# Kernel tuning notes

Measured on AMD Instinct MI355X. Metric: run time of the kernel, lower is better.

## Reference

```python
import jax, jax.numpy as jnp
import numpy as np
from math import sqrt

NUM_ENT = 100000
NUM_REL = 237  # base; rel table has 2*NUM_REL rows
DIM = 200
HALF = DIM // 2


def _lrelu(x, slope):
    return jnp.where(x >= 0, x, slope * x)


def setup_inputs() -> dict:
    key = jax.random.key(0)
    ks = jax.random.split(key, 20)
    s = 0.02
    inp = {
        'edge_index': jax.random.randint(ks[0], (2, 500000), 0, NUM_ENT),
        'edge_type': jax.random.randint(ks[1], (500000,), 0, 2 * NUM_REL),
        'toTest': jax.random.randint(ks[2], (131072, 2), 0, NUM_ENT),
        'ent_emb': s * jax.random.normal(ks[3], (NUM_ENT, DIM), jnp.float32),
        'rel_emb': s * jax.random.normal(ks[4], (2 * NUM_REL, DIM), jnp.float32),
        'W': s * jax.random.normal(ks[5], (DIM, DIM), jnp.float32),
        'W_loop': s * jax.random.normal(ks[6], (DIM, DIM), jnp.float32),
        'W_rel': s * jax.random.normal(ks[7], (DIM, DIM), jnp.float32),
        'trans_w': s * jax.random.normal(ks[8], (DIM, HALF), jnp.float32),
        'trans_b': jnp.zeros((HALF,), jnp.float32),
        'q_w': s * jax.random.normal(ks[9], (HALF, 128), jnp.float32),
        'q_b': jnp.zeros((128,), jnp.float32),
        'k_w': s * jax.random.normal(ks[10], (HALF, 128), jnp.float32),
        'k_b': jnp.zeros((128,), jnp.float32),
        'w1': s * jax.random.normal(ks[11], (DIM * 2 + 1 + 2 * NUM_REL, 2048), jnp.float32),
        'b1': jnp.zeros((2048,), jnp.float32),
        'w2': s * jax.random.normal(ks[12], (2048, 512), jnp.float32),
        'b2': jnp.zeros((512,), jnp.float32),
        'w3': s * jax.random.normal(ks[13], (512, 1), jnp.float32),
        'b3': jnp.zeros((1,), jnp.float32),
    }
    return inp


def reference(ent_emb, rel_emb, W, W_loop, W_rel, trans_w, trans_b,
              q_w, q_b, k_w, k_b, w1, b1, w2, b2, w3, b3,
              edge_index, edge_type, toTest):
    # --- CompGCN base layer ('sub' composition, degree-normalized scatter-add) ---
    src, dst = edge_index[0], edge_index[1]
    msg = (ent_emb[src] - rel_emb[edge_type]) @ W          # [E, D] gather + GEMM
    deg = jax.ops.segment_sum(jnp.ones_like(dst, jnp.float32), dst, num_segments=NUM_ENT)
    norm = jax.lax.rsqrt(jnp.maximum(deg, 1.0))
    agg = jax.ops.segment_sum(msg, dst, num_segments=NUM_ENT) * norm[:, None]
    all_ent = jnp.tanh(agg + ent_emb @ W_loop)             # [num_ent, D]
    all_rel = rel_emb @ W_rel                              # [2*num_rel, D]

    # --- PairRE test scoring path ---
    head_rel = all_rel[:, :HALF]                           # [2R, D/2]
    tail_rel = all_rel[:, HALF:]
    te = all_ent[toTest]                                   # [N, 2, D] gather
    ee = te @ trans_w + trans_b                            # [N, 2, D/2]
    h_e, t_e = ee[:, 0], ee[:, 1]
    atta = ((h_e @ q_w + q_b) * (t_e @ k_w + k_b)).sum(-1, keepdims=True) / sqrt(DIM)
    relSim = h_e @ head_rel.T - t_e @ tail_rel.T           # [N, 2R]
    cat = jnp.concatenate([te[:, 0], te[:, 1], atta, relSim], axis=1)
    h1 = _lrelu(cat @ w1 + b1, 1e-4)
    h2 = _lrelu(h1 @ w2 + b2, 1e-3)
    return jax.nn.sigmoid(h2 @ w3 + b3)                    # [N, 1]
```

## Files before the change

kernel.cpp:

```cpp
#include <hip/hip_runtime.h>

typedef unsigned short u16;
typedef unsigned long long u64;
typedef __attribute__((ext_vector_type(8))) short bf8;
typedef __attribute__((ext_vector_type(4))) float fx4;

#define N_ENT   100000
#define N_EDGE  500000
#define N_TEST  131072
#define EDIM    200
#define AE_LD   224
#define NB_SCAN 391

__device__ __forceinline__ u16 f2bf(float f) {
  union { float f; unsigned u; } c; c.f = f;
  return (u16)((c.u + 0x7FFFu + ((c.u >> 16) & 1u)) >> 16);
}
__device__ __forceinline__ float bf2f(u16 h) {
  union { unsigned u; float f; } c; c.u = ((unsigned)h) << 16;
  return c.f;
}
__device__ __forceinline__ void gload16(const u16* g, u16* l) {
  __builtin_amdgcn_global_load_lds(
      (const __attribute__((address_space(1))) void*)g,
      (__attribute__((address_space(3))) void*)l, 16, 0, 0);
}

#define BM 128
#define BN 128
#define BK 32
#define EPS 72

__global__ __launch_bounds__(256) void gemm_bf16(
    const u16* __restrict__ A, long lda,
    const u16* __restrict__ B, long ldb,
    u16* __restrict__ out, long ldOut,
    int K,
    const int* __restrict__ rowIdx, int idxMode, int mClamp,
    int mValid, int nValid, int nStore,
    const float* __restrict__ bias, int act, float slope,
    const u16* __restrict__ qbuf, const float* __restrict__ auxF,
    float* __restrict__ dotOut)
{
  __shared__ __align__(16) u16 smem[4 * 64 * EPS];
  u16* As = smem;
  u16* Bs = smem + BM * BK;
  const int tid  = threadIdx.x;
  const int wave = tid >> 6, lane = tid & 63;
  const int wr = (wave >> 1) * 64, wc = (wave & 1) * 64;
  const int fr = lane & 15, fq = lane >> 4;
  const long bm = (long)blockIdx.x * BM, bn = (long)blockIdx.y * BN;

  const int srow = wave * 32;
  const int kc = (lane & 3) * 8;
  long a0[2], a1[2], boff[2];
  #pragma unroll
  for (int h = 0; h < 2; ++h) {
    long gmRow = bm + srow + h * 16 + (lane >> 2);
    long b0, b1;
    if (idxMode == 0) {
      long gm = (gmRow >= mClamp) ? (mClamp - 1) : gmRow;
      b0 = gm * lda; b1 = b0;
    } else if (idxMode == 2) {
      b0 = (long)rowIdx[2 * gmRow] * lda; b1 = b0;
    } else if (idxMode == 3) {
      b0 = (long)rowIdx[2 * gmRow + 1] * lda; b1 = b0;
    } else {
      b0 = (long)rowIdx[2 * gmRow] * lda;
      b1 = (long)rowIdx[2 * gmRow + 1] * lda - 224;
    }
    a0[h] = b0 + kc; a1[h] = b1 + kc;
    boff[h] = (bn + srow + h * 16 + (lane >> 2)) * ldb + kc;
  }

  fx4 zero4 = {0.f, 0.f, 0.f, 0.f};
  fx4 acc[4][4];
  #pragma unroll
  for (int i = 0; i < 4; ++i)
    #pragma unroll
    for (int j = 0; j < 4; ++j) acc[i][j] = zero4;

  for (int k0 = 0; k0 < K; k0 += BK) {
    __syncthreads();
    const bool lo = (k0 + kc) < 224;
    #pragma unroll
    for (int h = 0; h < 2; ++h) {
      const long ao = (idxMode == 4) ? (lo ? a0[h] : a1[h]) : a0[h];
      gload16(A + ao + k0, &As[(srow + h * 16) * BK]);
      gload16(B + boff[h] + k0, &Bs[(srow + h * 16) * BK]);
    }
    __syncthreads();
    bf8 aF[4], bF[4];
    #pragma unroll
    for (int mt = 0; mt < 4; ++mt) aF[mt] = *(const bf8*)&As[(wr + mt * 16 + fr) * BK + fq * 8];
    #pragma unroll
    for (int nt = 0; nt < 4; ++nt) bF[nt] = *(const bf8*)&Bs[(wc + nt * 16 + fr) * BK + fq * 8];
    #pragma unroll
    for (int mt = 0; mt < 4; ++mt)
      #pragma unroll
      for (int nt = 0; nt < 4; ++nt)
        acc[mt][nt] = __builtin_amdgcn_mfma_f32_16x16x32_bf16(aF[mt], bF[nt], acc[mt][nt], 0, 0, 0);
  }

  if (act == 3 || act == 4) {
    #pragma unroll
    for (int mt = 0; mt < 4; ++mt) {
      #pragma unroll
      for (int r = 0; r < 4; ++r) {
        const long gm = bm + wr + mt * 16 + fq * 4 + r;
        float p = 0.f;
        #pragma unroll
        for (int nt = 0; nt < 4; ++nt) {
          const long gn = bn + wc + nt * 16 + fr;
          float v = acc[mt][nt][r] + bias[gn];
          if (act == 3) p += v * bf2f(qbuf[gm * 128 + gn]);
          else { v = (v >= 0.f) ? v : v * slope; p += v * auxF[gn]; }
        }
        p += __shfl_xor(p, 1, 64); p += __shfl_xor(p, 2, 64);
        p += __shfl_xor(p, 4, 64); p += __shfl_xor(p, 8, 64);
        if (fr == 0 && gm < mValid)
          atomicAdd(&dotOut[gm], (act == 3) ? p * 0.07071067811865475f : p);
      }
    }
    return;
  }

  __syncthreads();
  u16* ep = smem + wave * (64 * EPS);
  #pragma unroll
  for (int mt = 0; mt < 4; ++mt) {
    #pragma unroll
    for (int r = 0; r < 4; ++r) {
      const int lr = mt * 16 + fq * 4 + r;
      const long gm = bm + wr + lr;
      const float attaV = (act == 5) ? dotOut[gm] : 0.f;
      #pragma unroll
      for (int nt = 0; nt < 4; ++nt) {
        const long gn = bn + wc + nt * 16 + fr;
        float v = 0.f;
        if (gn < nValid) {
          v = acc[mt][nt][r];
          if (bias) v += bias[gn];
          if (act == 1) v = tanhf(v);
          else if (act == 5) { v += attaV * auxF[gn]; v = (v >= 0.f) ? v : v * slope; }
        }
        ep[lr * EPS + nt * 16 + fr] = f2bf(v);
      }
    }
  }
  #pragma unroll
  for (int it = 0; it < 8; ++it) {
    const int lr = it * 8 + (lane >> 3);
    const int lc = (lane & 7) * 8;
    const long gm = bm + wr + lr;
    const long gn = bn + wc + lc;
    if (gm < mValid && gn + 7 < nStore)
      *(bf8*)(out + gm * ldOut + gn) = *(const bf8*)&ep[lr * EPS + lc];
  }
}

__global__ void hist_kernel(const int* __restrict__ ei, int* __restrict__ cnt) {
  int e = blockIdx.x * 256 + threadIdx.x;
  if (e < N_EDGE) atomicAdd(&cnt[ei[N_EDGE + e]], 1);
}
__global__ void scanA_kernel(const int* __restrict__ cnt, int* __restrict__ offs,
                             int* __restrict__ blockSums) {
  __shared__ int s[256];
  int gid = blockIdx.x * 256 + threadIdx.x;
  int v = (gid < N_ENT) ? cnt[gid] : 0;
  s[threadIdx.x] = v;
  __syncthreads();
  for (int off = 1; off < 256; off <<= 1) {
    int t = (threadIdx.x >= off) ? s[threadIdx.x - off] : 0;
    __syncthreads();
    s[threadIdx.x] += t;
    __syncthreads();
  }
  if (gid < N_ENT) offs[gid] = s[threadIdx.x] - v;
  if (threadIdx.x == 255) blockSums[blockIdx.x] = s[255];
}
__global__ void scanB_kernel(const int* __restrict__ blockSums, int* __restrict__ blockOffs) {
  __shared__ int s[512];
  int v = (threadIdx.x < NB_SCAN) ? blockSums[threadIdx.x] : 0;
  s[threadIdx.x] = v;
  __syncthreads();
  for (int off = 1; off < 512; off <<= 1) {
    int t = (threadIdx.x >= off) ? s[threadIdx.x - off] : 0;
    __syncthreads();
    s[threadIdx.x] += t;
    __syncthreads();
  }
  if (threadIdx.x < NB_SCAN) blockOffs[threadIdx.x] = s[threadIdx.x] - v;
}
__global__ void scanC_kernel(int* __restrict__ offs, const int* __restrict__ blockOffs) {
  int gid = blockIdx.x * 256 + threadIdx.x;
  if (gid < N_ENT) offs[gid] += blockOffs[blockIdx.x];
}
__global__ void place_kernel(const int* __restrict__ ei, const int* __restrict__ et,
                             const int* __restrict__ offs, int* __restrict__ cursor,
                             int* __restrict__ sortedSrc, int* __restrict__ sortedT) {
  int e = blockIdx.x * 256 + threadIdx.x;
  if (e >= N_EDGE) return;
  int dst = ei[N_EDGE + e];
  int pos = offs[dst] + atomicAdd(&cursor[dst], 1);
  sortedSrc[pos] = ei[e];
  sortedT[pos]   = et[e];
}
__global__ void agg_A1_kernel(const int* __restrict__ offs, const int* __restrict__ cnt,
                              const int* __restrict__ sortedSrc, const int* __restrict__ sortedT,
                              const float* __restrict__ ent_emb, const float* __restrict__ rel_emb,
                              u16* __restrict__ A1) {
  const int r = blockIdx.x * 4 + (threadIdx.x >> 6);
  if (r >= N_ENT) return;
  const int lane = threadIdx.x & 63;
  const int beg = offs[r], n = cnt[r];
  u16* row = A1 + (size_t)r * 416;
  if (lane < 50) {
    float4 a = {0.f, 0.f, 0.f, 0.f};
    for (int e = 0; e < n; ++e) {
      const int s = sortedSrc[beg + e], t = sortedT[beg + e];
      float4 x = ((const float4*)(ent_emb + (size_t)s * EDIM))[lane];
      float4 y = ((const float4*)(rel_emb + (size_t)t * EDIM))[lane];
      a.x += x.x - y.x; a.y += x.y - y.y; a.z += x.z - y.z; a.w += x.w - y.w;
    }
    const float nm = rsqrtf(fmaxf((float)n, 1.f));
    u64 p = (u64)f2bf(a.x * nm) | ((u64)f2bf(a.y * nm) << 16)
          | ((u64)f2bf(a.z * nm) << 32) | ((u64)f2bf(a.w * nm) << 48);
    *(u64*)(row + 4 * lane) = p;
    float4 e = ((const float4*)(ent_emb + (size_t)r * EDIM))[lane];
    u64 q = (u64)f2bf(e.x) | ((u64)f2bf(e.y) << 16)
          | ((u64)f2bf(e.z) << 32) | ((u64)f2bf(e.w) << 48);
    *(u64*)(row + 200 + 4 * lane) = q;
  }
  if (lane < 16) row[400 + lane] = 0;
}

__global__ void build_B1T(const float* __restrict__ W, const float* __restrict__ W_loop,
                          u16* __restrict__ B1T)
{
  int idx = blockIdx.x * 256 + threadIdx.x;
  if (idx >= 256 * 416) return;
  int n = idx / 416, k = idx % 416;
  float v = 0.f;
  if (n < 200) {
    if (k < 200) v = W[k * 200 + n];
    else if (k < 400) v = W_loop[(k - 200) * 200 + n];
  }
  B1T[idx] = f2bf(v);
}
__global__ void all_rel_kernel(const float* __restrict__ rel_emb, const float* __restrict__ W_rel,
                               float* __restrict__ all_rel)
{
  int r = blockIdx.x, c = threadIdx.x;
  if (c >= 200) return;
  const float* re = rel_emb + r * 200;
  float a = 0.f;
  for (int k = 0; k < 200; ++k) a += re[k] * W_rel[k * 200 + c];
  all_rel[r * 200 + c] = a;
}
__global__ void pq_kernel(const float* __restrict__ all_rel, const float* __restrict__ w1,
                          float* __restrict__ PQ) {
  int idx = blockIdx.x * 256 + threadIdx.x;
  if (idx >= 2 * 100 * 2048) return;
  int n = idx & 2047, m = (idx >> 11) % 100, sel = idx / 204800;
  float a = 0.f;
  for (int r = 0; r < 474; ++r)
    a += all_rel[r * 200 + sel * 100 + m] * w1[(size_t)(401 + r) * 2048 + n];
  PQ[idx] = a;
}
__global__ void p2_kernel(const float* __restrict__ trans_w, const float* __restrict__ PQ,
                          float* __restrict__ P2) {
  int idx = blockIdx.x * 256 + threadIdx.x;
  if (idx >= 2 * 200 * 2048) return;
  int n = idx & 2047, k = (idx >> 11) % 200, sel = idx / 409600;
  const float* pq = PQ + sel * 204800;
  float a = 0.f;
  for (int m = 0; m < 100; ++m) a += trans_w[k * 100 + m] * pq[m * 2048 + n];
  P2[idx] = a;
}
__global__ void w1eff_kernel(const float* __restrict__ w1, const float* __restrict__ P2,
                             u16* __restrict__ W1eff) {
  int idx = blockIdx.x * 256 + threadIdx.x;
  if (idx >= 2048 * 448) return;
  int n = idx / 448, k = idx % 448;
  float v = 0.f;
  if (k < 200) v = w1[(size_t)k * 2048 + n] + P2[(size_t)k * 2048 + n];
  else if (k >= 224 && k < 424) {
    int kk = k - 224;
    v = w1[(size_t)(200 + kk) * 2048 + n] - P2[409600 + (size_t)kk * 2048 + n];
  }
  W1eff[idx] = f2bf(v);
}
__global__ void b1eff_kernel(const float* __restrict__ b1, const float* __restrict__ trans_b,
                             const float* __restrict__ PQ, float* __restrict__ b1eff) {
  int n = blockIdx.x * 256 + threadIdx.x;
  if (n >= 2048) return;
  float a = b1[n];
  for (int m = 0; m < 100; ++m)
    a += trans_b[m] * (PQ[m * 2048 + n] - PQ[204800 + m * 2048 + n]);
  b1eff[n] = a;
}
__global__ void qkw2_kernel(const float* __restrict__ trans_w, const float* __restrict__ q_w,
                            const float* __restrict__ k_w, u16* __restrict__ qw2T,
                            u16* __restrict__ kw2T) {
  int idx = blockIdx.x * 256 + threadIdx.x;
  if (idx >= 128 * 224) return;
  int j = idx / 224, k = idx % 224;
  float a = 0.f, b = 0.f;
  if (k < 200)
    for (int m = 0; m < 100; ++m) {
      float t = trans_w[k * 100 + m];
      a += t * q_w[m * 128 + j];
      b += t * k_w[m * 128 + j];
    }
  qw2T[idx] = f2bf(a);
  kw2T[idx] = f2bf(b);
}
__global__ void qkb2_kernel(const float* __restrict__ q_b, const float* __restrict__ k_b,
                            const float* __restrict__ trans_b, const float* __restrict__ q_w,
                            const float* __restrict__ k_w, float* __restrict__ qb2,
                            float* __restrict__ kb2) {
  int j = threadIdx.x;
  if (j >= 128) return;
  float a = q_b[j], b = k_b[j];
  for (int m = 0; m < 100; ++m) {
    a += trans_b[m] * q_w[m * 128 + j];
    b += trans_b[m] * k_w[m * 128 + j];
  }
  qb2[j] = a; kb2[j] = b;
}
__global__ void build_w2T(const float* __restrict__ w2, u16* __restrict__ w2T)
{
  long idx = (long)blockIdx.x * 256 + threadIdx.x;
  if (idx >= (long)512 * 2048) return;
  int n = (int)(idx / 2048), k = (int)(idx % 2048);
  w2T[idx] = f2bf(w2[(size_t)k * 512 + n]);
}
__global__ void sigmoid_kernel(const float* __restrict__ logit, const float* __restrict__ b3,
                               float* __restrict__ out) {
  int i = blockIdx.x * 256 + threadIdx.x;
  if (i >= N_TEST) return;
  out[i] = 1.f / (1.f + __expf(-(logit[i] + b3[0])));
}

extern "C" void kernel_launch(void* const* d_in, const int* in_sizes, int n_in,
                              void* d_out, int out_size, void* d_ws, size_t ws_size,
                              hipStream_t stream)
{
  (void)in_sizes; (void)n_in; (void)out_size;
  const int*   edge_index = (const int*)d_in[0];
  const int*   edge_type  = (const int*)d_in[1];
  const int*   toTest     = (const int*)d_in[2];
  const float* ent_emb    = (const float*)d_in[3];
  const float* rel_emb    = (const float*)d_in[4];
  const float* W          = (const float*)d_in[5];
  const float* W_loop     = (const float*)d_in[6];
  const float* W_rel      = (const float*)d_in[7];
  const float* trans_w    = (const float*)d_in[8];
  const float* trans_b    = (const float*)d_in[9];
  const float* q_w        = (const float*)d_in[10];
  const float* q_b        = (const float*)d_in[11];
  const float* k_w        = (const float*)d_in[12];
  const float* k_b        = (const float*)d_in[13];
  const float* w1         = (const float*)d_in[14];
  const float* b1         = (const float*)d_in[15];
  const float* w2         = (const float*)d_in[16];
  const float* b2         = (const float*)d_in[17];
  const float* w3         = (const float*)d_in[18];
  const float* b3         = (const float*)d_in[19];
  float* out = (float*)d_out;

  unsigned char* ws = (unsigned char*)d_ws;
  float* atta    = (float*)(ws + 0);
  float* logit   = (float*)(ws + 524288);
  float* allrel  = (float*)(ws + 1048576);
  u16*   B1T     = (u16*)  (ws + 1427968);
  u16*   W1eff   = (u16*)  (ws + 1640960);
  u16*   qw2T    = (u16*)  (ws + 3475968);
  u16*   kw2T    = (u16*)  (ws + 3533312);
  float* b1eff   = (float*)(ws + 3590656);
  float* qb2     = (float*)(ws + 3598848);
  float* kb2     = (float*)(ws + 3599872);
  u16*   w2T     = (u16*)  (ws + 3600896);
  const size_t X_base = 5698048;
  u16*   all_ent = (u16*)  (ws + X_base);
  u16*   Qbuf    = (u16*)  (ws + X_base + 44800000);
  const size_t Y_base = 84052480;
  u16*   A1      = (u16*)  (ws + Y_base);
  const size_t Z_base = 167252480;

  int*   cnt       = (int*)  (ws + Z_base);
  int*   offs      = (int*)  (ws + Z_base + 400000);
  int*   cursor    = (int*)  (ws + Z_base + 800000);
  int*   blockSums = (int*)  (ws + Z_base + 1200000);
  int*   blockOffs = (int*)  (ws + Z_base + 1202048);
  int*   sortedSrc = (int*)  (ws + Z_base + 1204096);
  int*   sortedT   = (int*)  (ws + Z_base + 3204096);
  float* PQ        = (float*)(ws + Z_base + 5204096);
  float* P2        = (float*)(ws + Z_base + 6842496);

  int CH;
  if      (Z_base + (size_t)131072 * 4096 <= ws_size) CH = 131072;
  else if (Z_base + (size_t)65536  * 4096 <= ws_size) CH = 65536;
  else if (Z_base + (size_t)32768  * 4096 <= ws_size) CH = 32768;
  else if (Z_base + (size_t)16384  * 4096 <= ws_size) CH = 16384;
  else if (Z_base + (size_t)8192   * 4096 <= ws_size) CH = 8192;
  else return;
  u16* h1 = (u16*)(ws + Z_base);
  const int NC = N_TEST / CH;

  hipMemsetAsync(cnt, 0, 400000, stream);
  hipMemsetAsync(cursor, 0, 400000, stream);
  hipMemsetAsync(atta, 0, 524288, stream);
  hipMemsetAsync(logit, 0, 524288, stream);

  hist_kernel<<<(N_EDGE + 255) / 256, 256, 0, stream>>>(edge_index, cnt);
  scanA_kernel<<<NB_SCAN, 256, 0, stream>>>(cnt, offs, blockSums);
  scanB_kernel<<<1, 512, 0, stream>>>(blockSums, blockOffs);
  scanC_kernel<<<NB_SCAN, 256, 0, stream>>>(offs, blockOffs);
  place_kernel<<<(N_EDGE + 255) / 256, 256, 0, stream>>>(edge_index, edge_type, offs, cursor,
                                                         sortedSrc, sortedT);
  agg_A1_kernel<<<(N_ENT + 3) / 4, 256, 0, stream>>>(offs, cnt, sortedSrc, sortedT,
                                                     ent_emb, rel_emb, A1);
  build_B1T<<<(256 * 416) / 256, 256, 0, stream>>>(W, W_loop, B1T);

  gemm_bf16<<<dim3(782, 2), 256, 0, stream>>>(A1, 416, B1T, 416, all_ent, AE_LD,
      416, nullptr, 0, N_ENT, N_ENT, 200, AE_LD, nullptr, 1, 0.f, nullptr, nullptr, nullptr);

  all_rel_kernel<<<474, 256, 0, stream>>>(rel_emb, W_rel, allrel);
  pq_kernel<<<(2 * 100 * 2048) / 256, 256, 0, stream>>>(allrel, w1, PQ);
  p2_kernel<<<(2 * 200 * 2048) / 256, 256, 0, stream>>>(trans_w, PQ, P2);
  w1eff_kernel<<<(2048 * 448) / 256, 256, 0, stream>>>(w1, P2, W1eff);
  b1eff_kernel<<<8, 256, 0, stream>>>(b1, trans_b, PQ, b1eff);
  qkw2_kernel<<<(128 * 224) / 256, 256, 0, stream>>>(trans_w, q_w, k_w, qw2T, kw2T);
  qkb2_kernel<<<1, 128, 0, stream>>>(q_b, k_b, trans_b, q_w, k_w, qb2, kb2);
  build_w2T<<<(512 * 2048) / 256, 256, 0, stream>>>(w2, w2T);

  gemm_bf16<<<dim3(1024, 1), 256, 0, stream>>>(all_ent, AE_LD, qw2T, AE_LD, Qbuf, 128,
      AE_LD, toTest, 2, 0, N_TEST, 128, 128, qb2, 0, 0.f, nullptr, nullptr, nullptr);
  gemm_bf16<<<dim3(1024, 1), 256, 0, stream>>>(all_ent, AE_LD, kw2T, AE_LD, nullptr, 0,
      AE_LD, toTest, 3, 0, N_TEST, 128, 128, kb2, 3, 0.f, Qbuf, nullptr, atta);

  for (int c = 0; c < NC; ++c) {
    gemm_bf16<<<dim3(CH / 128, 16), 256, 0, stream>>>(all_ent, AE_LD, W1eff, 448, h1, 2048,
        448, toTest + (size_t)c * CH * 2, 4, 0, CH, 2048, 2048, b1eff, 5, 0.0001f,
        nullptr, w1 + (size_t)400 * 2048, atta + (size_t)c * CH);
    gemm_bf16<<<dim3(CH / 128, 4), 256, 0, stream>>>(h1, 2048, w2T, 2048, nullptr, 0,
        2048, nullptr, 0, CH, CH, 512, 512, b2, 4, 0.001f,
        nullptr, w3, logit + (size_t)c * CH);
  }
  sigmoid_kernel<<<N_TEST / 256, 256, 0, stream>>>(logit, b3, out);
}
```

Measured before the change: 1.832 ms.

## Template GEMM tile size to 256x256 blocks and XOR-swizzle LDS layout

Turns the bf16 MFMA GEMM into a template over the per-wave M tiles and the waves along N. The large GEMMs now run 256x256 tiles on 512-thread blocks, which raises operand reuse per LDS load and halves the grid. It also XOR-swizzles the K-chunk slot used for global-to-LDS writes and fragment reads to cut LDS bank conflicts. The epilogue is restaged in 32-row pieces to fit the per-wave LDS budget. The costs are higher register pressure from 8x4 accumulators (lower occupancy) and fewer blocks for the first GEMM (391 for 100k rows).

```diff
diff --git a/kernel.cpp b/kernel.cpp
--- a/kernel.cpp
+++ b/kernel.cpp
@@ -26,12 +26,11 @@
       (__attribute__((address_space(3))) void*)l, 16, 0, 0);
 }
 
-#define BM 128
-#define BN 128
 #define BK 32
 #define EPS 72
 
-__global__ __launch_bounds__(256) void gemm_bf16(
+template<int TM, int WN>
+__global__ __launch_bounds__(64 * 2 * WN) void gemm_t(
     const u16* __restrict__ A, long lda,
     const u16* __restrict__ B, long ldb,
     u16* __restrict__ out, long ldOut,
@@ -42,17 +41,20 @@
     const u16* __restrict__ qbuf, const float* __restrict__ auxF,
     float* __restrict__ dotOut)
 {
-  __shared__ __align__(16) u16 smem[4 * 64 * EPS];
+  constexpr int BM = TM * 32;
+  constexpr int BN = WN * 64;
+  constexpr int WAVES = 2 * WN;
+  __shared__ __align__(16) u16 smem[WAVES * 32 * EPS];
   u16* As = smem;
   u16* Bs = smem + BM * BK;
   const int tid  = threadIdx.x;
   const int wave = tid >> 6, lane = tid & 63;
-  const int wr = (wave >> 1) * 64, wc = (wave & 1) * 64;
+  const int wr = (wave / WN) * (TM * 16), wc = (wave % WN) * 64;
   const int fr = lane & 15, fq = lane >> 4;
   const long bm = (long)blockIdx.x * BM, bn = (long)blockIdx.y * BN;
 
   const int srow = wave * 32;
-  const int kc = (lane & 3) * 8;
+  const int kc = (((lane & 3) ^ ((lane >> 3) & 3)) * 8);
   long a0[2], a1[2], boff[2];
   #pragma unroll
   for (int h = 0; h < 2; ++h) {
@@ -74,9 +76,9 @@
   }
 
   fx4 zero4 = {0.f, 0.f, 0.f, 0.f};
-  fx4 acc[4][4];
+  fx4 acc[TM][4];
   #pragma unroll
-  for (int i = 0; i < 4; ++i)
+  for (int i = 0; i < TM; ++i)
     #pragma unroll
     for (int j = 0; j < 4; ++j) acc[i][j] = zero4;
 
@@ -90,13 +92,16 @@
       gload16(B + boff[h] + k0, &Bs[(srow + h * 16) * BK]);
     }
     __syncthreads();
-    bf8 aF[4], bF[4];
-    #pragma unroll
-    for (int mt = 0; mt < 4; ++mt) aF[mt] = *(const bf8*)&As[(wr + mt * 16 + fr) * BK + fq * 8];
-    #pragma unroll
-    for (int nt = 0; nt < 4; ++nt) bF[nt] = *(const bf8*)&Bs[(wc + nt * 16 + fr) * BK + fq * 8];
-    #pragma unroll
-    for (int mt = 0; mt < 4; ++mt)
+    bf8 aF[TM], bF[4];
+    const int rslot = (fq ^ ((fr >> 1) & 3)) * 8;
+    #pragma unroll
+    for (int mt = 0; mt < TM; ++mt)
+      aF[mt] = *(const bf8*)&As[(wr + mt * 16 + fr) * BK + rslot];
+    #pragma unroll
+    for (int nt = 0; nt < 4; ++nt)
+      bF[nt] = *(const bf8*)&Bs[(wc + nt * 16 + fr) * BK + rslot];
+    #pragma unroll
+    for (int mt = 0; mt < TM; ++mt)
       #pragma unroll
       for (int nt = 0; nt < 4; ++nt)
         acc[mt][nt] = __builtin_amdgcn_mfma_f32_16x16x32_bf16(aF[mt], bF[nt], acc[mt][nt], 0, 0, 0);
@@ -104,7 +109,7 @@
 
   if (act == 3 || act == 4) {
     #pragma unroll
-    for (int mt = 0; mt < 4; ++mt) {
+    for (int mt = 0; mt < TM; ++mt) {
       #pragma unroll
       for (int r = 0; r < 4; ++r) {
         const long gm = bm + wr + mt * 16 + fq * 4 + r;
@@ -126,36 +131,40 @@
   }
 
   __syncthreads();
-  u16* ep = smem + wave * (64 * EPS);
+  u16* ep = smem + wave * (32 * EPS);
   #pragma unroll
-  for (int mt = 0; mt < 4; ++mt) {
-    #pragma unroll
-    for (int r = 0; r < 4; ++r) {
-      const int lr = mt * 16 + fq * 4 + r;
-      const long gm = bm + wr + lr;
-      const float attaV = (act == 5) ? dotOut[gm] : 0.f;
+  for (int p = 0; p < TM / 2; ++p) {
+    #pragma unroll
+    for (int mt2 = 0; mt2 < 2; ++mt2) {
+      const int mt = 2 * p + mt2;
       #pragma unroll
-      for (int nt = 0; nt < 4; ++nt) {
-        const long gn = bn + wc + nt * 16 + fr;
-        float v = 0.f;
-        if (gn < nValid) {
-          v = acc[mt][nt][r];
-          if (bias) v += bias[gn];
-          if (act == 1) v = tanhf(v);
-          else if (act == 5) { v += attaV * auxF[gn]; v = (v >= 0.f) ? v : v * slope; }
+      for (int r = 0; r < 4; ++r) {
+        const int lrl = mt2 * 16 + fq * 4 + r;
+        const long gm = bm + wr + mt * 16 + fq * 4 + r;
+        const float attaV = (act == 5) ? dotOut[gm] : 0.f;
+        #pragma unroll
+        for (int nt = 0; nt < 4; ++nt) {
+          const long gn = bn + wc + nt * 16 + fr;
+          float v = 0.f;
+          if (gn < nValid) {
+            v = acc[mt][nt][r];
+            if (bias) v += bias[gn];
+            if (act == 1) v = tanhf(v);
+            else if (act == 5) { v += attaV * auxF[gn]; v = (v >= 0.f) ? v : v * slope; }
+          }
+          ep[lrl * EPS + nt * 16 + fr] = f2bf(v);
         }
-        ep[lr * EPS + nt * 16 + fr] = f2bf(v);
       }
     }
-  }
-  #pragma unroll
-  for (int it = 0; it < 8; ++it) {
-    const int lr = it * 8 + (lane >> 3);
-    const int lc = (lane & 7) * 8;
-    const long gm = bm + wr + lr;
-    const long gn = bn + wc + lc;
-    if (gm < mValid && gn + 7 < nStore)
-      *(bf8*)(out + gm * ldOut + gn) = *(const bf8*)&ep[lr * EPS + lc];
+    #pragma unroll
+    for (int it = 0; it < 4; ++it) {
+      const int lr = it * 8 + (lane >> 3);
+      const int lc = (lane & 7) * 8;
+      const long gm = bm + wr + p * 32 + lr;
+      const long gn = bn + wc + lc;
+      if (gm < mValid && gn + 7 < nStore)
+        *(bf8*)(out + gm * ldOut + gn) = *(const bf8*)&ep[lr * EPS + lc];
+    }
   }
 }
 
@@ -424,7 +433,7 @@
                                                      ent_emb, rel_emb, A1);
   build_B1T<<<(256 * 416) / 256, 256, 0, stream>>>(W, W_loop, B1T);
 
-  gemm_bf16<<<dim3(782, 2), 256, 0, stream>>>(A1, 416, B1T, 416, all_ent, AE_LD,
+  gemm_t<8, 4><<<dim3(391, 1), 512, 0, stream>>>(A1, 416, B1T, 416, all_ent, AE_LD,
       416, nullptr, 0, N_ENT, N_ENT, 200, AE_LD, nullptr, 1, 0.f, nullptr, nullptr, nullptr);
 
   all_rel_kernel<<<474, 256, 0, stream>>>(rel_emb, W_rel, allrel);
@@ -436,16 +445,16 @@
   qkb2_kernel<<<1, 128, 0, stream>>>(q_b, k_b, trans_b, q_w, k_w, qb2, kb2);
   build_w2T<<<(512 * 2048) / 256, 256, 0, stream>>>(w2, w2T);
 
-  gemm_bf16<<<dim3(1024, 1), 256, 0, stream>>>(all_ent, AE_LD, qw2T, AE_LD, Qbuf, 128,
+  gemm_t<4, 2><<<dim3(1024, 1), 256, 0, stream>>>(all_ent, AE_LD, qw2T, AE_LD, Qbuf, 128,
       AE_LD, toTest, 2, 0, N_TEST, 128, 128, qb2, 0, 0.f, nullptr, nullptr, nullptr);
-  gemm_bf16<<<dim3(1024, 1), 256, 0, stream>>>(all_ent, AE_LD, kw2T, AE_LD, nullptr, 0,
+  gemm_t<4, 2><<<dim3(1024, 1), 256, 0, stream>>>(all_ent, AE_LD, kw2T, AE_LD, nullptr, 0,
       AE_LD, toTest, 3, 0, N_TEST, 128, 128, kb2, 3, 0.f, Qbuf, nullptr, atta);
 
   for (int c = 0; c < NC; ++c) {
-    gemm_bf16<<<dim3(CH / 128, 16), 256, 0, stream>>>(all_ent, AE_LD, W1eff, 448, h1, 2048,
+    gemm_t<8, 4><<<dim3(CH / 256, 8), 512, 0, stream>>>(all_ent, AE_LD, W1eff, 448, h1, 2048,
         448, toTest + (size_t)c * CH * 2, 4, 0, CH, 2048, 2048, b1eff, 5, 0.0001f,
         nullptr, w1 + (size_t)400 * 2048, atta + (size_t)c * CH);
-    gemm_bf16<<<dim3(CH / 128, 4), 256, 0, stream>>>(h1, 2048, w2T, 2048, nullptr, 0,
+    gemm_t<8, 4><<<dim3(CH / 256, 2), 512, 0, stream>>>(h1, 2048, w2T, 2048, nullptr, 0,
         2048, nullptr, 0, CH, CH, 512, 512, b2, 4, 0.001f,
         nullptr, w3, logit + (size_t)c * CH);
   }
```

After: 1.876 ms. +2.5%, slower.
